# Optimization experiments

Measured on AMD Instinct MI355X. Metric: run time of the kernel, lower is better.

The kernel has to match this reference:

```python
import jax, jax.numpy as jnp
import numpy as np

B, T, C, H = 4, 2048, 1024, 16
HD = C // H  # head dim = 64


def setup_inputs() -> dict:
    key = jax.random.key(0)
    ks = jax.random.split(key, 9)
    s = 1.0 / np.sqrt(C)
    return {
        "x": jax.random.normal(ks[0], (B, T, C), dtype=jnp.float32),
        "Wq": jax.random.normal(ks[1], (C, C), dtype=jnp.float32) * s,
        "bq": jnp.zeros((C,), dtype=jnp.float32),
        "Wk": jax.random.normal(ks[2], (C, C), dtype=jnp.float32) * s,
        "bk": jnp.zeros((C,), dtype=jnp.float32),
        "Wv": jax.random.normal(ks[3], (C, C), dtype=jnp.float32) * s,
        "bv": jnp.zeros((C,), dtype=jnp.float32),
        "Wo": jax.random.normal(ks[4], (C, C), dtype=jnp.float32) * s,
        "bo": jnp.zeros((C,), dtype=jnp.float32),
    }


def reference(x, Wq, bq, Wk, bk, Wv, bv, Wo, bo):
    # Linear projections (torch Linear: x @ W.T + b)
    q = x @ Wq.T + bq
    k = x @ Wk.T + bk
    v = x @ Wv.T + bv
    # [B, T, C] -> [B, H, T, HD]
    def split(t):
        return t.reshape(B, T, H, HD).transpose(0, 2, 1, 3)
    q, k, v = split(q), split(k), split(v)
    scores = jnp.einsum("bhqd,bhkd->bhqk", q, k) / np.sqrt(HD).astype(np.float32)
    causal = jnp.tril(jnp.ones((T, T), dtype=bool))
    scores = jnp.where(causal[None, None], scores, -jnp.inf)
    attn = jax.nn.softmax(scores, axis=-1)
    # dropout layers are identity in eval mode
    out = jnp.einsum("bhqk,bhkd->bhqd", attn, v)
    out = out.transpose(0, 2, 1, 3).reshape(B, T, C)
    return out @ Wo.T + bo
```

## Files before the change

### kernel.cpp

```cpp
#include <hip/hip_runtime.h>
#include <hip/hip_bf16.h>

#define DEVI __device__ __forceinline__

typedef __attribute__((ext_vector_type(4))) float f32x4;
typedef __attribute__((ext_vector_type(8))) short bf16x8;
typedef __attribute__((ext_vector_type(4))) short bf16x4;

constexpr int Bb = 4, Tt = 2048, Cc = 1024, Hh = 16, HDd = 64;
constexpr int Mm = Bb * Tt;

DEVI short f2bf(float f) {
    union { float f; unsigned u; } x; x.f = f;
    unsigned r = x.u + 0x7FFFu + ((x.u >> 16) & 1u);
    return (short)(r >> 16);
}

DEVI int cvtpk(float lo, float hi) {
    int r;
    asm("v_cvt_pk_bf16_f32 %0, %1, %2" : "=v"(r) : "v"(lo), "v"(hi));
    return r;
}

DEVI void gload_lds16(const void* g, void* l) {
    __builtin_amdgcn_global_load_lds(
        (const __attribute__((address_space(1))) unsigned int*)g,
        (__attribute__((address_space(3))) unsigned int*)l, 16, 0, 0);
}

__global__ void cvt_kernel(const float* __restrict__ s, short* __restrict__ d, int n8) {
    int i = blockIdx.x * 256 + threadIdx.x;
    if (i < n8) {
        const float4* sp = (const float4*)s;
        float4 a = sp[2 * i], b = sp[2 * i + 1];
        short tmp[8];
        tmp[0] = f2bf(a.x); tmp[1] = f2bf(a.y); tmp[2] = f2bf(a.z); tmp[3] = f2bf(a.w);
        tmp[4] = f2bf(b.x); tmp[5] = f2bf(b.y); tmp[6] = f2bf(b.z); tmp[7] = f2bf(b.w);
        *(bf16x8*)(d + 8 * (size_t)i) = *(bf16x8*)tmp;
    }
}

__global__ void cvtw_kernel(const float* __restrict__ w0, const float* __restrict__ w1,
                            const float* __restrict__ w2, const float* __restrict__ w3,
                            short* __restrict__ d0, short* __restrict__ d1,
                            short* __restrict__ d2, short* __restrict__ d3) {
    const int sel = blockIdx.y;
    const float* s = sel == 0 ? w0 : sel == 1 ? w1 : sel == 2 ? w2 : w3;
    short* d = sel == 0 ? d0 : sel == 1 ? d1 : sel == 2 ? d2 : d3;
    const int i = blockIdx.x * 256 + threadIdx.x;
    const float4* sp = (const float4*)s;
    float4 a = sp[2 * i], b = sp[2 * i + 1];
    short tmp[8];
    tmp[0] = f2bf(a.x); tmp[1] = f2bf(a.y); tmp[2] = f2bf(a.z); tmp[3] = f2bf(a.w);
    tmp[4] = f2bf(b.x); tmp[5] = f2bf(b.y); tmp[6] = f2bf(b.z); tmp[7] = f2bf(b.w);
    *(bf16x8*)(d + 8 * (size_t)i) = *(bf16x8*)tmp;
}

struct GemmAcc { f32x4 acc[4][4]; };

DEVI void gemm_core(const short* __restrict__ A, const short* __restrict__ Bw,
                    int Kdim, int bm, int bn, int tid,
                    short (*As)[64], short (*Bs)[64], GemmAcc& G)
{
    const int lane = tid & 63, wid = tid >> 6;
    const int wr = wid >> 1, wc = wid & 1;
    const int lrow = lane >> 3;
    const int lcol = (lane & 7) * 8;

    for (int k0 = 0; k0 < Kdim; k0 += 64) {
        #pragma unroll
        for (int c = 0; c < 4; ++c) {
            const int chunk = wid * 4 + c;
            const int row = chunk * 8 + lrow;
            gload_lds16(A  + (size_t)(bm + row) * Kdim + k0 + lcol, &As[chunk * 8][0]);
            gload_lds16(Bw + (size_t)(bn + row) * Kdim + k0 + lcol, &Bs[chunk * 8][0]);
        }
        __syncthreads();
        const int rr = lane & 15;
        #pragma unroll
        for (int kk = 0; kk < 64; kk += 32) {
            const int koff = kk + (lane >> 4) * 8;
            bf16x8 af[4], bfr[4];
            #pragma unroll
            for (int m_ = 0; m_ < 4; ++m_)
                af[m_] = *(const bf16x8*)&As[wr * 64 + m_ * 16 + rr][koff];
            #pragma unroll
            for (int n_ = 0; n_ < 4; ++n_)
                bfr[n_] = *(const bf16x8*)&Bs[wc * 64 + n_ * 16 + rr][koff];
            #pragma unroll
            for (int m_ = 0; m_ < 4; ++m_)
                #pragma unroll
                for (int n_ = 0; n_ < 4; ++n_)
                    G.acc[m_][n_] = __builtin_amdgcn_mfma_f32_16x16x32_bf16(
                        af[m_], bfr[n_], G.acc[m_][n_], 0, 0, 0);
        }
        __syncthreads();
    }
}

__global__ __launch_bounds__(256, 2)
void gemm_qkv(const short* __restrict__ A,
              const short* __restrict__ Wq, const short* __restrict__ Wk,
              const short* __restrict__ Wv,
              const float* __restrict__ bq, const float* __restrict__ bk,
              const float* __restrict__ bv,
              short* __restrict__ Qo, short* __restrict__ Ko, short* __restrict__ Vto,
              float sq)
{
    __shared__ __align__(16) short As[128][64];
    __shared__ __align__(16) short Bs[128][64];
    const int sec = blockIdx.y >> 3;
    const int bn = (blockIdx.y & 7) * 128;
    const int bm = blockIdx.x * 128;
    const short* Bw = sec == 0 ? Wq : sec == 1 ? Wk : Wv;
    const float* bias = sec == 0 ? bq : sec == 1 ? bk : bv;
    const float scale = sec == 0 ? sq : 1.0f;

    GemmAcc G = {};
    gemm_core(A, Bw, Cc, bm, bn, threadIdx.x, As, Bs, G);

    const int lane = threadIdx.x & 63, wid = threadIdx.x >> 6;
    const int wr = wid >> 1, wc = wid & 1;
    const int cidx = lane & 15;
    const int r4 = (lane >> 4) * 4;
    #pragma unroll
    for (int n_ = 0; n_ < 4; ++n_) {
        const int col = bn + wc * 64 + n_ * 16 + cidx;
        const float bv_ = bias[col];
        #pragma unroll
        for (int m_ = 0; m_ < 4; ++m_) {
            const int rowb = bm + wr * 64 + m_ * 16 + r4;
            if (sec == 2) {
                const int h_ = col >> 6, d_ = col & 63;
                const int b_ = rowb >> 11, t_ = rowb & 2047;
                short tmp[4];
                #pragma unroll
                for (int i = 0; i < 4; ++i) tmp[i] = f2bf((G.acc[m_][n_][i] + bv_));
                *(bf16x4*)(Vto + ((size_t)((b_ * Hh + h_) * HDd + d_)) * Tt + t_) = *(bf16x4*)tmp;
            } else {
                short* C = sec == 0 ? Qo : Ko;
                #pragma unroll
                for (int i = 0; i < 4; ++i)
                    C[(size_t)(rowb + i) * Cc + col] = f2bf((G.acc[m_][n_][i] + bv_) * scale);
            }
        }
    }
}

__global__ __launch_bounds__(256, 2)
void gemm_out(const short* __restrict__ A, const short* __restrict__ Bw,
              const float* __restrict__ bias, float* __restrict__ Cout)
{
    __shared__ __align__(16) short As[128][64];
    __shared__ __align__(16) short Bs[128][64];
    const int bm = blockIdx.x * 128;
    const int bn = blockIdx.y * 128;
    GemmAcc G = {};
    gemm_core(A, Bw, Cc, bm, bn, threadIdx.x, As, Bs, G);

    const int lane = threadIdx.x & 63, wid = threadIdx.x >> 6;
    const int wr = wid >> 1, wc = wid & 1;
    const int cidx = lane & 15;
    const int r4 = (lane >> 4) * 4;
    #pragma unroll
    for (int n_ = 0; n_ < 4; ++n_) {
        const int col = bn + wc * 64 + n_ * 16 + cidx;
        const float bv_ = bias[col];
        #pragma unroll
        for (int m_ = 0; m_ < 4; ++m_) {
            const int rowb = bm + wr * 64 + m_ * 16 + r4;
            #pragma unroll
            for (int i = 0; i < 4; ++i)
                Cout[(size_t)(rowb + i) * Cc + col] = G.acc[m_][n_][i] + bv_;
        }
    }
}

template<bool DIAG>
DEVI void attn_tile(int kv0, const short (*Kt)[64], const short (*Vd)[64],
                    bf16x8 qf0, bf16x8 qf1, int lane, short (*PsW)[64],
                    f32x4 (&oacc)[4], float &mrow, float &lsum, int qrow)
{
    const int rr = lane & 15;
    const int g  = lane >> 4;

    f32x4 sacc[4] = {};
    __builtin_amdgcn_s_setprio(1);
    #pragma unroll
    for (int n = 0; n < 4; ++n) {
        const int row = n * 16 + rr;
        const int sw = row & 7;
        bf16x8 kf0 = *(const bf16x8*)&Kt[row][((g    ) ^ sw) * 8];
        bf16x8 kf1 = *(const bf16x8*)&Kt[row][((g + 4) ^ sw) * 8];
        sacc[n] = __builtin_amdgcn_mfma_f32_16x16x32_bf16(kf0, qf0, sacc[n], 0, 0, 0);
        sacc[n] = __builtin_amdgcn_mfma_f32_16x16x32_bf16(kf1, qf1, sacc[n], 0, 0, 0);
    }
    __builtin_amdgcn_s_setprio(0);

    float p[4][4];
    float pmax = -1e30f;
    #pragma unroll
    for (int n = 0; n < 4; ++n)
        #pragma unroll
        for (int i = 0; i < 4; ++i) {
            float s = sacc[n][i];
            if (DIAG) { if (kv0 + n * 16 + g * 4 + i > qrow) s = -1e30f; }
            p[n][i] = s;
            pmax = fmaxf(pmax, s);
        }
    pmax = fmaxf(pmax, __shfl_xor(pmax, 16, 64));
    pmax = fmaxf(pmax, __shfl_xor(pmax, 32, 64));

    if (!__all(pmax <= mrow + 8.0f)) {
        const float mnew = fmaxf(mrow, pmax);
        const float alpha = exp2f(mrow - mnew);
        mrow = mnew;
        lsum *= alpha;
        float alphaq[4];
        #pragma unroll
        for (int i = 0; i < 4; ++i) alphaq[i] = __shfl(alpha, g * 4 + i, 16);
        #pragma unroll
        for (int n = 0; n < 4; ++n)
            #pragma unroll
            for (int i = 0; i < 4; ++i) oacc[n][i] *= alphaq[i];
    }

    #pragma unroll
    for (int n = 0; n < 4; ++n) {
        #pragma unroll
        for (int i = 0; i < 4; ++i) {
            p[n][i] = exp2f(p[n][i] - mrow);
            lsum += p[n][i];
        }
        const unsigned u0 = (unsigned)cvtpk(p[n][0], p[n][1]);
        const unsigned u1 = (unsigned)cvtpk(p[n][2], p[n][3]);
        const int chunk = (2 * n + (g >> 1)) ^ (rr & 7);
        *(unsigned long long*)&PsW[rr][chunk * 8 + (g & 1) * 4] =
            ((unsigned long long)u1 << 32) | u0;
    }

    #pragma unroll
    for (int ks = 0; ks < 2; ++ks) {
        const int rchunk = (4 * ks + g) ^ (rr & 7);
        bf16x8 pf = *(const bf16x8*)&PsW[rr][rchunk * 8];
        __builtin_amdgcn_s_setprio(1);
        #pragma unroll
        for (int n = 0; n < 4; ++n) {
            const int row = n * 16 + rr;
            const int sw = row & 7;
            bf16x8 vf = *(const bf16x8*)&Vd[row][((ks * 4 + g) ^ sw) * 8];
            oacc[n] = __builtin_amdgcn_mfma_f32_16x16x32_bf16(pf, vf, oacc[n], 0, 0, 0);
        }
        __builtin_amdgcn_s_setprio(0);
    }
}

DEVI void attn_run(int qt, const short* __restrict__ Q, short* __restrict__ O,
                   const short* kbase, const short* vbase, size_t baseRow, int h,
                   int lane, int wid,
                   short (*Kb)[64][64], short (*Vb)[64][64], short (*PsW)[64])
{
    const int q0 = qt * 128;
    const int rr = lane & 15;
    const int g = lane >> 4;

    const int qrow = q0 + wid * 16 + rr;
    const short* qptr = Q + (baseRow + qrow) * Cc + h * HDd + g * 8;
    bf16x8 qf0 = *(const bf16x8*)qptr;
    bf16x8 qf1 = *(const bf16x8*)(qptr + 32);

    f32x4 oacc[4] = {};
    float mrow = -1e30f, lsum = 0.f;
    const int NT = 2 * qt + 2;

    auto STAGE = [&](int bsel, int kv0) {
        const int r0 = wid * 8;
        const int row = r0 + (lane >> 3);
        const int sc = ((lane & 7) ^ (row & 7)) * 8;
        gload_lds16(kbase + (size_t)(kv0 + row) * Cc + sc, &Kb[bsel][r0][0]);
        gload_lds16(vbase + (size_t)row * Tt + kv0 + sc, &Vb[bsel][r0][0]);
    };

    STAGE(0, 0);
    int buf = 0;
    for (int kt = 0; kt < NT; ++kt) {
        if (kt + 1 < NT) {
            STAGE(buf ^ 1, (kt + 1) * 64);
            asm volatile("s_waitcnt vmcnt(2)" ::: "memory");
        } else {
            asm volatile("s_waitcnt vmcnt(0)" ::: "memory");
        }
        __builtin_amdgcn_s_barrier();
        __builtin_amdgcn_sched_barrier(0);
        if (kt >= NT - 2)
            attn_tile<true >(kt * 64, Kb[buf], Vb[buf], qf0, qf1, lane, PsW, oacc, mrow, lsum, qrow);
        else
            attn_tile<false>(kt * 64, Kb[buf], Vb[buf], qf0, qf1, lane, PsW, oacc, mrow, lsum, qrow);
        __builtin_amdgcn_s_barrier();
        buf ^= 1;
    }

    lsum += __shfl_xor(lsum, 16, 64);
    lsum += __shfl_xor(lsum, 32, 64);
    float rinv[4];
    #pragma unroll
    for (int i = 0; i < 4; ++i)
        rinv[i] = 1.0f / __shfl(lsum, g * 4 + i, 16);

    #pragma unroll
    for (int n = 0; n < 4; ++n)
        #pragma unroll
        for (int i = 0; i < 4; ++i)
            O[(baseRow + q0 + wid * 16 + g * 4 + i) * Cc + h * HDd + n * 16 + rr] =
                f2bf(oacc[n][i] * rinv[i]);
}

__global__ __launch_bounds__(512, 2)
void attn_kernel(const short* __restrict__ Q, const short* __restrict__ K,
                 const short* __restrict__ Vt, short* __restrict__ O)
{
    const int bh = blockIdx.y;
    const int b = bh >> 4, h = bh & 15;
    const size_t baseRow = (size_t)b * Tt;
    const int tid = threadIdx.x, lane = tid & 63, wid = tid >> 6;

    __shared__ __align__(16) short Kb[2][64][64];
    __shared__ __align__(16) short Vb[2][64][64];
    __shared__ __align__(16) short Ps[8][16][64];
    short (*PsW)[64] = Ps[wid];

    const short* kbase = K + baseRow * Cc + h * HDd;
    const short* vbase = Vt + (size_t)bh * HDd * Tt;

    const int qtA = blockIdx.x;
    const int qtB = (Tt / 128 - 1) - blockIdx.x;

    attn_run(qtB, Q, O, kbase, vbase, baseRow, h, lane, wid, Kb, Vb, PsW);
    attn_run(qtA, Q, O, kbase, vbase, baseRow, h, lane, wid, Kb, Vb, PsW);
}

extern "C" void kernel_launch(void* const* d_in, const int* in_sizes, int n_in,
                              void* d_out, int out_size, void* d_ws, size_t ws_size,
                              hipStream_t stream) {
    (void)in_sizes; (void)n_in; (void)out_size; (void)ws_size;
    const float* x  = (const float*)d_in[0];
    const float* Wq = (const float*)d_in[1];
    const float* bq = (const float*)d_in[2];
    const float* Wk = (const float*)d_in[3];
    const float* bk = (const float*)d_in[4];
    const float* Wv = (const float*)d_in[5];
    const float* bv = (const float*)d_in[6];
    const float* Wo = (const float*)d_in[7];
    const float* bo = (const float*)d_in[8];
    float* out = (float*)d_out;

    short* ws  = (short*)d_ws;
    short* xb  = ws;
    short* wqb = xb  + (size_t)Mm * Cc;
    short* wkb = wqb + (size_t)Cc * Cc;
    short* wvb = wkb + (size_t)Cc * Cc;
    short* wob = wvb + (size_t)Cc * Cc;
    short* Qb  = wob + (size_t)Cc * Cc;
    short* Kbg = Qb  + (size_t)Mm * Cc;
    short* Vtb = Kbg + (size_t)Mm * Cc;
    short* Ob  = Vtb + (size_t)Mm * Cc;

    const int nx8 = Mm * Cc / 8;
    const int nw8 = Cc * Cc / 8;
    cvt_kernel<<<(nx8 + 255) / 256, 256, 0, stream>>>(x, xb, nx8);
    cvtw_kernel<<<dim3(nw8 / 256, 4), 256, 0, stream>>>(Wq, Wk, Wv, Wo, wqb, wkb, wvb, wob);

    const float SCL = 0.125f * 1.44269504088896f;
    gemm_qkv<<<dim3(Mm / 128, 24), 256, 0, stream>>>(xb, wqb, wkb, wvb, bq, bk, bv,
                                                     Qb, Kbg, Vtb, SCL);

    attn_kernel<<<dim3(Tt / 256, Bb * Hh), 512, 0, stream>>>(Qb, Kbg, Vtb, Ob);

    gemm_out<<<dim3(Mm / 128, Cc / 128), 256, 0, stream>>>(Ob, wob, bo, out);
}
```

Baseline: 188.4 us.

## Switch attention to 32x32 MFMA with in-register P via permlane swap

Rewrites the attention tile to use 32x32x16 bf16 MFMA, with each wave owning 32 query rows and 4 waves per block instead of 8. The P matrix is repacked into the A-operand layout in registers with v_permlane32_swap, which removes the per-wave LDS scratch buffer and its write/read round trip. K/V staging now issues two loads per thread. The change trades more registers per wave (f32x16 accumulators) and fewer waves per block for fewer LDS transactions and fewer MFMA issues per tile.

```diff
diff --git a/kernel.cpp b/kernel.cpp
--- a/kernel.cpp
+++ b/kernel.cpp
@@ -4,6 +4,7 @@
 #define DEVI __device__ __forceinline__
 
 typedef __attribute__((ext_vector_type(4))) float f32x4;
+typedef __attribute__((ext_vector_type(16))) float f32x16;
 typedef __attribute__((ext_vector_type(8))) short bf16x8;
 typedef __attribute__((ext_vector_type(4))) short bf16x4;
 
@@ -178,37 +179,38 @@
 
 template<bool DIAG>
 DEVI void attn_tile(int kv0, const short (*Kt)[64], const short (*Vd)[64],
-                    bf16x8 qf0, bf16x8 qf1, int lane, short (*PsW)[64],
-                    f32x4 (&oacc)[4], float &mrow, float &lsum, int qrow)
-{
-    const int rr = lane & 15;
-    const int g  = lane >> 4;
-
-    f32x4 sacc[4] = {};
+                    const bf16x8 (&qf)[4], int lane, int qrow,
+                    f32x16 (&oacc)[2], float &mrow, float &lsum)
+{
+    const int q31 = lane & 31;
+    const int hi  = lane >> 5;
+
+    f32x16 sacc[2] = {};
     __builtin_amdgcn_s_setprio(1);
     #pragma unroll
-    for (int n = 0; n < 4; ++n) {
-        const int row = n * 16 + rr;
-        const int sw = row & 7;
-        bf16x8 kf0 = *(const bf16x8*)&Kt[row][((g    ) ^ sw) * 8];
-        bf16x8 kf1 = *(const bf16x8*)&Kt[row][((g + 4) ^ sw) * 8];
-        sacc[n] = __builtin_amdgcn_mfma_f32_16x16x32_bf16(kf0, qf0, sacc[n], 0, 0, 0);
-        sacc[n] = __builtin_amdgcn_mfma_f32_16x16x32_bf16(kf1, qf1, sacc[n], 0, 0, 0);
+    for (int ks = 0; ks < 4; ++ks) {
+        #pragma unroll
+        for (int nb = 0; nb < 2; ++nb) {
+            const int row = nb * 32 + q31;
+            bf16x8 kf = *(const bf16x8*)&Kt[row][(((ks << 1) | hi) ^ (row & 7)) * 8];
+            sacc[nb] = __builtin_amdgcn_mfma_f32_32x32x16_bf16(kf, qf[ks], sacc[nb], 0, 0, 0);
+        }
     }
     __builtin_amdgcn_s_setprio(0);
 
-    float p[4][4];
     float pmax = -1e30f;
     #pragma unroll
-    for (int n = 0; n < 4; ++n)
-        #pragma unroll
-        for (int i = 0; i < 4; ++i) {
-            float s = sacc[n][i];
-            if (DIAG) { if (kv0 + n * 16 + g * 4 + i > qrow) s = -1e30f; }
-            p[n][i] = s;
+    for (int nb = 0; nb < 2; ++nb)
+        #pragma unroll
+        for (int r = 0; r < 16; ++r) {
+            float s = sacc[nb][r];
+            if (DIAG) {
+                const int kv = kv0 + nb * 32 + (r & 3) + 8 * (r >> 2) + 4 * hi;
+                if (kv > qrow) s = -1e30f;
+            }
+            sacc[nb][r] = s;
             pmax = fmaxf(pmax, s);
         }
-    pmax = fmaxf(pmax, __shfl_xor(pmax, 16, 64));
     pmax = fmaxf(pmax, __shfl_xor(pmax, 32, 64));
 
     if (!__all(pmax <= mrow + 8.0f)) {
@@ -216,40 +218,40 @@
         const float alpha = exp2f(mrow - mnew);
         mrow = mnew;
         lsum *= alpha;
-        float alphaq[4];
-        #pragma unroll
-        for (int i = 0; i < 4; ++i) alphaq[i] = __shfl(alpha, g * 4 + i, 16);
-        #pragma unroll
-        for (int n = 0; n < 4; ++n)
-            #pragma unroll
-            for (int i = 0; i < 4; ++i) oacc[n][i] *= alphaq[i];
-    }
-
-    #pragma unroll
-    for (int n = 0; n < 4; ++n) {
-        #pragma unroll
-        for (int i = 0; i < 4; ++i) {
-            p[n][i] = exp2f(p[n][i] - mrow);
-            lsum += p[n][i];
-        }
-        const unsigned u0 = (unsigned)cvtpk(p[n][0], p[n][1]);
-        const unsigned u1 = (unsigned)cvtpk(p[n][2], p[n][3]);
-        const int chunk = (2 * n + (g >> 1)) ^ (rr & 7);
-        *(unsigned long long*)&PsW[rr][chunk * 8 + (g & 1) * 4] =
-            ((unsigned long long)u1 << 32) | u0;
-    }
-
-    #pragma unroll
-    for (int ks = 0; ks < 2; ++ks) {
-        const int rchunk = (4 * ks + g) ^ (rr & 7);
-        bf16x8 pf = *(const bf16x8*)&PsW[rr][rchunk * 8];
+        #pragma unroll
+        for (int r = 0; r < 16; ++r) {
+            const float ar = __shfl(alpha, (r & 3) + 8 * (r >> 2) + 4 * hi, 32);
+            oacc[0][r] *= ar;
+            oacc[1][r] *= ar;
+        }
+    }
+
+    #pragma unroll
+    for (int nb = 0; nb < 2; ++nb)
+        #pragma unroll
+        for (int r = 0; r < 16; ++r) {
+            const float pe = exp2f(sacc[nb][r] - mrow);
+            sacc[nb][r] = pe;
+            lsum += pe;
+        }
+
+    #pragma unroll
+    for (int ks = 0; ks < 4; ++ks) {
+        const int n = ks >> 1, b8 = (ks & 1) * 8;
+        int x0 = cvtpk(sacc[n][b8 + 0], sacc[n][b8 + 1]);
+        int x1 = cvtpk(sacc[n][b8 + 2], sacc[n][b8 + 3]);
+        int y0 = cvtpk(sacc[n][b8 + 4], sacc[n][b8 + 5]);
+        int y1 = cvtpk(sacc[n][b8 + 6], sacc[n][b8 + 7]);
+        asm volatile("v_permlane32_swap_b32 %0, %1" : "+v"(x0), "+v"(y0));
+        asm volatile("v_permlane32_swap_b32 %0, %1" : "+v"(x1), "+v"(y1));
+        union { int w[4]; bf16x8 v; } pa;
+        pa.w[0] = x0; pa.w[1] = x1; pa.w[2] = y0; pa.w[3] = y1;
         __builtin_amdgcn_s_setprio(1);
         #pragma unroll
-        for (int n = 0; n < 4; ++n) {
-            const int row = n * 16 + rr;
-            const int sw = row & 7;
-            bf16x8 vf = *(const bf16x8*)&Vd[row][((ks * 4 + g) ^ sw) * 8];
-            oacc[n] = __builtin_amdgcn_mfma_f32_16x16x32_bf16(pf, vf, oacc[n], 0, 0, 0);
+        for (int nb = 0; nb < 2; ++nb) {
+            const int row = nb * 32 + q31;
+            bf16x8 vf = *(const bf16x8*)&Vd[row][(((ks << 1) | hi) ^ (row & 7)) * 8];
+            oacc[nb] = __builtin_amdgcn_mfma_f32_32x32x16_bf16(pa.v, vf, oacc[nb], 0, 0, 0);
         }
         __builtin_amdgcn_s_setprio(0);
     }
@@ -257,28 +259,31 @@
 
 DEVI void attn_run(int qt, const short* __restrict__ Q, short* __restrict__ O,
                    const short* kbase, const short* vbase, size_t baseRow, int h,
-                   int lane, int wid,
-                   short (*Kb)[64][64], short (*Vb)[64][64], short (*PsW)[64])
+                   int lane, int wid, short (*Kb)[64][64], short (*Vb)[64][64])
 {
     const int q0 = qt * 128;
-    const int rr = lane & 15;
-    const int g = lane >> 4;
-
-    const int qrow = q0 + wid * 16 + rr;
-    const short* qptr = Q + (baseRow + qrow) * Cc + h * HDd + g * 8;
-    bf16x8 qf0 = *(const bf16x8*)qptr;
-    bf16x8 qf1 = *(const bf16x8*)(qptr + 32);
-
-    f32x4 oacc[4] = {};
+    const int q31 = lane & 31;
+    const int hi = lane >> 5;
+    const int qrow = q0 + wid * 32 + q31;
+
+    const short* qptr = Q + (baseRow + qrow) * Cc + h * HDd + hi * 8;
+    bf16x8 qf[4];
+    #pragma unroll
+    for (int ks = 0; ks < 4; ++ks) qf[ks] = *(const bf16x8*)(qptr + ks * 16);
+
+    f32x16 oacc[2] = {};
     float mrow = -1e30f, lsum = 0.f;
     const int NT = 2 * qt + 2;
 
     auto STAGE = [&](int bsel, int kv0) {
-        const int r0 = wid * 8;
-        const int row = r0 + (lane >> 3);
-        const int sc = ((lane & 7) ^ (row & 7)) * 8;
-        gload_lds16(kbase + (size_t)(kv0 + row) * Cc + sc, &Kb[bsel][r0][0]);
-        gload_lds16(vbase + (size_t)row * Tt + kv0 + sc, &Vb[bsel][r0][0]);
+        #pragma unroll
+        for (int j = 0; j < 2; ++j) {
+            const int r0 = wid * 16 + j * 8;
+            const int row = r0 + (lane >> 3);
+            const int sc = ((lane & 7) ^ (row & 7)) * 8;
+            gload_lds16(kbase + (size_t)(kv0 + row) * Cc + sc, &Kb[bsel][r0][0]);
+            gload_lds16(vbase + (size_t)row * Tt + kv0 + sc, &Vb[bsel][r0][0]);
+        }
     };
 
     STAGE(0, 0);
@@ -286,36 +291,32 @@
     for (int kt = 0; kt < NT; ++kt) {
         if (kt + 1 < NT) {
             STAGE(buf ^ 1, (kt + 1) * 64);
-            asm volatile("s_waitcnt vmcnt(2)" ::: "memory");
+            asm volatile("s_waitcnt vmcnt(4)" ::: "memory");
         } else {
             asm volatile("s_waitcnt vmcnt(0)" ::: "memory");
         }
         __builtin_amdgcn_s_barrier();
         __builtin_amdgcn_sched_barrier(0);
         if (kt >= NT - 2)
-            attn_tile<true >(kt * 64, Kb[buf], Vb[buf], qf0, qf1, lane, PsW, oacc, mrow, lsum, qrow);
+            attn_tile<true >(kt * 64, Kb[buf], Vb[buf], qf, lane, qrow, oacc, mrow, lsum);
         else
-            attn_tile<false>(kt * 64, Kb[buf], Vb[buf], qf0, qf1, lane, PsW, oacc, mrow, lsum, qrow);
+            attn_tile<false>(kt * 64, Kb[buf], Vb[buf], qf, lane, qrow, oacc, mrow, lsum);
         __builtin_amdgcn_s_barrier();
         buf ^= 1;
     }
 
-    lsum += __shfl_xor(lsum, 16, 64);
     lsum += __shfl_xor(lsum, 32, 64);
-    float rinv[4];
-    #pragma unroll
-    for (int i = 0; i < 4; ++i)
-        rinv[i] = 1.0f / __shfl(lsum, g * 4 + i, 16);
-
-    #pragma unroll
-    for (int n = 0; n < 4; ++n)
-        #pragma unroll
-        for (int i = 0; i < 4; ++i)
-            O[(baseRow + q0 + wid * 16 + g * 4 + i) * Cc + h * HDd + n * 16 + rr] =
-                f2bf(oacc[n][i] * rinv[i]);
-}
-
-__global__ __launch_bounds__(512, 2)
+    #pragma unroll
+    for (int r = 0; r < 16; ++r) {
+        const int crow = (r & 3) + 8 * (r >> 2) + 4 * hi;
+        const float ri = 1.0f / __shfl(lsum, crow, 32);
+        const size_t rb = (baseRow + q0 + wid * 32 + crow) * Cc + h * HDd + q31;
+        O[rb]      = f2bf(oacc[0][r] * ri);
+        O[rb + 32] = f2bf(oacc[1][r] * ri);
+    }
+}
+
+__global__ __launch_bounds__(256, 4)
 void attn_kernel(const short* __restrict__ Q, const short* __restrict__ K,
                  const short* __restrict__ Vt, short* __restrict__ O)
 {
@@ -326,8 +327,6 @@
 
     __shared__ __align__(16) short Kb[2][64][64];
     __shared__ __align__(16) short Vb[2][64][64];
-    __shared__ __align__(16) short Ps[8][16][64];
-    short (*PsW)[64] = Ps[wid];
 
     const short* kbase = K + baseRow * Cc + h * HDd;
     const short* vbase = Vt + (size_t)bh * HDd * Tt;
@@ -335,8 +334,8 @@
     const int qtA = blockIdx.x;
     const int qtB = (Tt / 128 - 1) - blockIdx.x;
 
-    attn_run(qtB, Q, O, kbase, vbase, baseRow, h, lane, wid, Kb, Vb, PsW);
-    attn_run(qtA, Q, O, kbase, vbase, baseRow, h, lane, wid, Kb, Vb, PsW);
+    attn_run(qtB, Q, O, kbase, vbase, baseRow, h, lane, wid, Kb, Vb);
+    attn_run(qtA, Q, O, kbase, vbase, baseRow, h, lane, wid, Kb, Vb);
 }
 
 extern "C" void kernel_launch(void* const* d_in, const int* in_sizes, int n_in,
@@ -374,7 +373,7 @@
     gemm_qkv<<<dim3(Mm / 128, 24), 256, 0, stream>>>(xb, wqb, wkb, wvb, bq, bk, bv,
                                                      Qb, Kbg, Vtb, SCL);
 
-    attn_kernel<<<dim3(Tt / 256, Bb * Hh), 512, 0, stream>>>(Qb, Kbg, Vtb, Ob);
+    attn_kernel<<<dim3(Tt / 256, Bb * Hh), 256, 0, stream>>>(Qb, Kbg, Vtb, Ob);
 
     gemm_out<<<dim3(Mm / 128, Cc / 128), 256, 0, stream>>>(Ob, wob, bo, out);
 }
```

New measurement: 218.5 us. +16.0%, slower.
